# Performance work log

Measured on AMD Instinct MI355X. Metric: run time of the kernel, lower is better.

Reference implementation:

```python
import jax, jax.numpy as jnp
import numpy as np

GRAPH_SIZE = 100000  # == N, used as scalar multiplier on Q


def setup_inputs() -> dict:
    key = jax.random.key(0)
    ks = jax.random.split(key, 10)
    N, D, K, C, S = 100000, 128, 10, 50000, 100
    inp = {
        "seeds_idx_pad": jax.random.randint(ks[0], (1, S), 0, N + 1),  # N = pad row
        "seeds_idx_num": jnp.full((1, 1), 50.0, dtype=jnp.float32),
        "candidates_idx": jax.random.randint(ks[1], (C,), 0, N),
        "all_nodes": jnp.arange(N),
        "mask": jnp.ones((N, 1), dtype=jnp.float32),
        "features": jax.random.normal(ks[2], (N, D), dtype=jnp.float32),
        "neigh_idx": jax.random.randint(ks[3], (N, K), 0, N),
        "W_self": jax.random.normal(ks[4], (D, D), dtype=jnp.float32) * 0.05,
        "W_neigh": jax.random.normal(ks[5], (D, D), dtype=jnp.float32) * 0.05,
        "W1": jax.random.normal(ks[6], (D, D + 1), dtype=jnp.float32) * 0.05,
        "W2": jax.random.normal(ks[7], (D, D + 1), dtype=jnp.float32) * 0.05,
        "W3": jax.random.normal(ks[8], (D, D + 1), dtype=jnp.float32) * 0.05,
    }
    return inp


def _sage(features, neigh_idx, all_nodes, mask, W_self, W_neigh):
    x = features[all_nodes]                 # [N, D]
    nb_mean = features[neigh_idx].mean(axis=1)  # [N, K, D] -> [N, D]
    h = jax.nn.relu(x @ W_self + nb_mean @ W_neigh)
    return h * mask                          # [N, D]


def reference(seeds_idx_pad, seeds_idx_num, candidates_idx, all_nodes, mask,
              features, neigh_idx, W_self, W_neigh, W1, W2, W3):
    D = features.shape[1]
    embedding = _sage(features, neigh_idx, all_nodes, mask, W_self, W_neigh)  # [N, D]
    embedding_pad = jnp.concatenate([embedding, jnp.zeros((1, D), embedding.dtype)], axis=0)
    seeds_emb = embedding_pad[seeds_idx_pad]                  # [1, S, D]
    seeds_mean = jax.nn.sigmoid((seeds_emb.sum(axis=1) / seeds_idx_num) @ W1)  # [1, D+1]
    global_mean = jax.nn.sigmoid(embedding.mean(axis=0)[None, :] @ W2)         # computed but unused, as in source
    candi_emb = jax.nn.sigmoid(embedding[candidates_idx] @ W3)                 # [C, D+1]
    Q = (1.0 - jnp.sum(candi_emb * seeds_mean, axis=1)) * GRAPH_SIZE           # [C]
    return Q
```

## Files before the change

### kernel.cpp

```cpp
#include <hip/hip_runtime.h>

#define D     128
#define DP1   129
#define KN    10
#define GSZ   100000.0f

typedef __attribute__((ext_vector_type(8))) _Float16 f16x8;
typedef __attribute__((ext_vector_type(4))) float f32x4;
typedef __attribute__((ext_vector_type(4))) unsigned uintx4;

#define MFMA16(a, b, c) __builtin_amdgcn_mfma_f32_16x16x32_f16((a), (b), (c), 0, 0, 0)

__device__ __forceinline__ float sigmoidf_(float x) {
    return 1.0f / (1.0f + __expf(-x));
}

__global__ __launch_bounds__(256) void prep_kernel(
    const float* __restrict__ features,
    const float* __restrict__ Wself, const float* __restrict__ Wneigh,
    const float* __restrict__ W3,
    const int*   __restrict__ seeds,
    const float* __restrict__ mask,
    const int*   __restrict__ neigh,
    unsigned short* __restrict__ featb,
    unsigned short* __restrict__ W2T,
    unsigned short* __restrict__ W3T,
    float*          __restrict__ srow,
    int N, int S, int doW)
{
    int b = blockIdx.x;
    const int t = threadIdx.x;

    if (b < S) {
        const int node = seeds[b];
        if (node >= N || node < 0) {
            if (t < D) srow[b * D + t] = 0.f;
            return;
        }
        __shared__ float xs[D], nb[D];
        if (t < D) {
            xs[t] = features[(size_t)node * D + t];
            float a = 0.f;
            #pragma unroll
            for (int k = 0; k < KN; ++k)
                a += features[(size_t)neigh[node * KN + k] * D + t];
            nb[t] = a * (1.0f / KN);
        }
        __syncthreads();
        if (t < D) {
            float h = 0.f;
            #pragma unroll 4
            for (int dp = 0; dp < D; ++dp)
                h = fmaf(xs[dp], Wself[dp * D + t],
                         fmaf(nb[dp], Wneigh[dp * D + t], h));
            srow[b * D + t] = fmaxf(h, 0.f) * mask[node];
        }
        return;
    }
    b -= S;

    if (b < doW * 200) {
        const int u = b * 256 + t;
        if (u < 128 * 256) {
            int n = u >> 8, k = u & 255;
            float v = (k < 128) ? Wself[k * 128 + n] : Wneigh[(k - 128) * 128 + n];
            W2T[n * 256 + k] = __builtin_bit_cast(unsigned short, (_Float16)v);
        } else {
            int w = u - 128 * 256;
            if (w < 144 * 128) {
                int j = w >> 7, k = w & 127;
                float v = (j < DP1) ? W3[k * DP1 + j] : 0.0f;
                W3T[j * 128 + k] = __builtin_bit_cast(unsigned short, (_Float16)v);
            }
        }
        return;
    }
    b -= doW * 200;

    const int i = b * 256 + t;
    const int n8 = N * (D / 8);
    if (i < n8) {
        const float4 a = *(const float4*)(features + (size_t)i * 8);
        const float4 c = *(const float4*)(features + (size_t)i * 8 + 4);
        f16x8 v;
        v[0] = (_Float16)a.x; v[1] = (_Float16)a.y;
        v[2] = (_Float16)a.z; v[3] = (_Float16)a.w;
        v[4] = (_Float16)c.x; v[5] = (_Float16)c.y;
        v[6] = (_Float16)c.z; v[7] = (_Float16)c.w;
        *(f16x8*)(featb + (size_t)i * 8) = v;
    }
}

__global__ __launch_bounds__(256) void sm_kernel(
    const float* __restrict__ srow, int S,
    const float* __restrict__ snum,
    const float* __restrict__ W1,
    float*       __restrict__ smp)
{
    __shared__ float ps[2][D];
    __shared__ float s[D];
    const int t   = threadIdx.x;
    const int col = t & 127;
    const int hf  = t >> 7;
    float a = 0.f;
    for (int b = hf; b < S; b += 2) a += srow[b * D + col];
    ps[hf][col] = a;
    __syncthreads();
    if (t < D) s[t] = (ps[0][t] + ps[1][t]) / snum[0];
    __syncthreads();
    if (t < DP1) {
        float acc = 0.f;
        #pragma unroll 4
        for (int dp = 0; dp < D; ++dp)
            acc = fmaf(s[dp], W1[dp * DP1 + t], acc);
        smp[t] = sigmoidf_(acc);
    } else if (t < 144) {
        smp[t] = 0.0f;
    }
}

__global__ __launch_bounds__(256, 2) void fused_kernel(
    const int*            __restrict__ cand,
    const float*          __restrict__ mask,
    const unsigned short* __restrict__ featb,
    const int*            __restrict__ neigh,
    const unsigned short* __restrict__ W2T,
    const unsigned short* __restrict__ W3T,
    const float*          __restrict__ smp,
    float*                __restrict__ Q,
    int C)
{
    __shared__ unsigned short tile[16][256];
    __shared__ float msk[16];
    __shared__ float qred[4][16];

    const int lane  = threadIdx.x & 63;
    const int wv    = threadIdx.x >> 6;
    const int cbase = blockIdx.x * 16;

    const int g   = lane >> 4;
    const int n15 = lane & 15;

    {
        const int L   = lane & 15;
        const int grp = lane >> 4;
        const int m   = wv * 4 + grp;
        const int cc  = cbase + m;
        const int nd  = cand[(cc < C) ? cc : 0];
        if (L == 0) msk[m] = (cc < C) ? mask[nd] : 0.f;

        int rix[KN];
        #pragma unroll
        for (int k = 0; k < KN; ++k) rix[k] = neigh[nd * KN + k];

        const uintx4 xv = *(const uintx4*)(featb + (size_t)nd * D + L * 8);
        uintx4 vr[KN];
        #pragma unroll
        for (int k = 0; k < KN; ++k)
            vr[k] = *(const uintx4*)(featb + (size_t)rix[k] * D + L * 8);

        f16x8 s8 = __builtin_bit_cast(f16x8, vr[0]);
        #pragma unroll
        for (int k = 1; k < KN; ++k)
            s8 += __builtin_bit_cast(f16x8, vr[k]);
        const f16x8 nb8 = s8 * (f16x8)((_Float16)(1.0f / KN));

        const int sw = (m & 7) << 3;
        unsigned short* tw = &tile[0][0];
        *(uintx4*)(tw + m * 256 + ((L * 8) ^ sw))       = xv;
        *(uintx4*)(tw + m * 256 + ((128 + L * 8) ^ sw)) = __builtin_bit_cast(uintx4, nb8);
    }

    const int swr = (n15 & 7) << 3;
    const unsigned short* tp = &tile[0][0];

    __syncthreads();

    f16x8 afr[8];
    #pragma unroll
    for (int ks = 0; ks < 8; ++ks)
        afr[ks] = *reinterpret_cast<const f16x8*>(tp + n15 * 256 + ((ks * 32 + g * 8) ^ swr));

    f32x4 acc1[2];
    acc1[0] = (f32x4){0.f, 0.f, 0.f, 0.f};
    acc1[1] = (f32x4){0.f, 0.f, 0.f, 0.f};

    #pragma unroll
    for (int ks = 0; ks < 8; ++ks) {
        #pragma unroll
        for (int i = 0; i < 2; ++i) {
            const f16x8 b = *reinterpret_cast<const f16x8*>(
                W2T + ((wv * 2 + i) * 16 + n15) * 256 + ks * 32 + g * 8);
            acc1[i] = MFMA16(afr[ks], b, acc1[i]);
        }
    }

    float mr[4];
    #pragma unroll
    for (int r = 0; r < 4; ++r) mr[r] = msk[g * 4 + r];

    __syncthreads();

    #pragma unroll
    for (int i = 0; i < 2; ++i) {
        const f32x4 v = acc1[i];
        #pragma unroll
        for (int r = 0; r < 4; ++r) {
            const int m2 = g * 4 + r;
            tile[m2][(((wv * 2 + i) * 16 + n15)) ^ ((m2 & 7) << 3)] =
                __builtin_bit_cast(unsigned short, (_Float16)(fmaxf(v[r], 0.f) * mr[r]));
        }
    }
    __syncthreads();

    f16x8 ah[4];
    #pragma unroll
    for (int ks = 0; ks < 4; ++ks)
        ah[ks] = *reinterpret_cast<const f16x8*>(tp + n15 * 256 + ((ks * 32 + g * 8) ^ swr));

    const int jt0 = wv, jt1 = 4 + wv;
    f32x4 acc2[3];
    acc2[0] = (f32x4){0.f, 0.f, 0.f, 0.f};
    acc2[1] = (f32x4){0.f, 0.f, 0.f, 0.f};
    acc2[2] = (f32x4){0.f, 0.f, 0.f, 0.f};

    #pragma unroll
    for (int ks = 0; ks < 4; ++ks) {
        const f16x8 b0 = *reinterpret_cast<const f16x8*>(
            W3T + (jt0 * 16 + n15) * 128 + ks * 32 + g * 8);
        acc2[0] = MFMA16(ah[ks], b0, acc2[0]);
        const f16x8 b1 = *reinterpret_cast<const f16x8*>(
            W3T + (jt1 * 16 + n15) * 128 + ks * 32 + g * 8);
        acc2[1] = MFMA16(ah[ks], b1, acc2[1]);
        if (wv == 0) {
            const f16x8 b2 = *reinterpret_cast<const f16x8*>(
                W3T + (8 * 16 + n15) * 128 + ks * 32 + g * 8);
            acc2[2] = MFMA16(ah[ks], b2, acc2[2]);
        }
    }

    float qp[4] = {0.f, 0.f, 0.f, 0.f};
    {
        const float sm0 = smp[jt0 * 16 + n15];
        const float sm1 = smp[jt1 * 16 + n15];
        #pragma unroll
        for (int r = 0; r < 4; ++r) {
            qp[r] += sm0 * sigmoidf_(acc2[0][r]);
            qp[r] += sm1 * sigmoidf_(acc2[1][r]);
        }
        if (wv == 0) {
            const float sm2 = smp[8 * 16 + n15];
            #pragma unroll
            for (int r = 0; r < 4; ++r)
                qp[r] += sm2 * sigmoidf_(acc2[2][r]);
        }
    }
    #pragma unroll
    for (int off = 8; off >= 1; off >>= 1)
        #pragma unroll
        for (int r = 0; r < 4; ++r)
            qp[r] += __shfl_xor(qp[r], off);

    if (n15 == 0) {
        #pragma unroll
        for (int r = 0; r < 4; ++r)
            qred[wv][g * 4 + r] = qp[r];
    }
    __syncthreads();

    const int t = threadIdx.x;
    if (t < 16) {
        const float s = qred[0][t] + qred[1][t] + qred[2][t] + qred[3][t];
        const int cr = cbase + t;
        if (cr < C) Q[cr] = (1.0f - s) * GSZ;
    }
}

#define MCAND 8
__global__ __launch_bounds__(128) void cand_kernel(
    const int*   __restrict__ cand,
    const float* __restrict__ mask,
    const float* __restrict__ features,
    const int*   __restrict__ neigh,
    const float* __restrict__ Wself,
    const float* __restrict__ Wneigh,
    const float* __restrict__ W3,
    const float* __restrict__ sm,
    float*       __restrict__ Q,
    int C)
{
    const int c0 = blockIdx.x * MCAND;
    const int t  = threadIdx.x;

    __shared__ float z[2 * MCAND][D];
    __shared__ float h[MCAND][D];
    __shared__ float red1[MCAND][D];
    __shared__ float red2[MCAND][D];
    __shared__ float smsh[DP1];

    smsh[t] = sm[t];
    if (t == 0) smsh[D] = sm[D];

    float mskv[MCAND];
    #pragma unroll
    for (int m = 0; m < MCAND; ++m) {
        const int c    = c0 + m;
        const int node = (c < C) ? cand[c] : cand[0];
        mskv[m] = mask[node];
        z[m][t] = features[(size_t)node * D + t];
        float a = 0.f;
        #pragma unroll
        for (int k = 0; k < KN; ++k)
            a += features[(size_t)neigh[node * KN + k] * D + t];
        z[MCAND + m][t] = a * (1.0f / KN);
    }
    __syncthreads();

    float acc[MCAND];
    #pragma unroll
    for (int m = 0; m < MCAND; ++m) acc[m] = 0.f;
    for (int dp = 0; dp < D; dp += 4) {
        const float ws0 = Wself[(dp + 0) * D + t];
        const float ws1 = Wself[(dp + 1) * D + t];
        const float ws2 = Wself[(dp + 2) * D + t];
        const float ws3 = Wself[(dp + 3) * D + t];
        const float wn0 = Wneigh[(dp + 0) * D + t];
        const float wn1 = Wneigh[(dp + 1) * D + t];
        const float wn2 = Wneigh[(dp + 2) * D + t];
        const float wn3 = Wneigh[(dp + 3) * D + t];
        #pragma unroll
        for (int m = 0; m < MCAND; ++m) {
            const float4 xv = *(const float4*)&z[m][dp];
            const float4 nv = *(const float4*)&z[MCAND + m][dp];
            float a = acc[m];
            a = fmaf(xv.x, ws0, a); a = fmaf(xv.y, ws1, a);
            a = fmaf(xv.z, ws2, a); a = fmaf(xv.w, ws3, a);
            a = fmaf(nv.x, wn0, a); a = fmaf(nv.y, wn1, a);
            a = fmaf(nv.z, wn2, a); a = fmaf(nv.w, wn3, a);
            acc[m] = a;
        }
    }
    #pragma unroll
    for (int m = 0; m < MCAND; ++m)
        h[m][t] = fmaxf(acc[m], 0.f) * mskv[m];
    __syncthreads();

    #pragma unroll
    for (int m = 0; m < MCAND; ++m) acc[m] = 0.f;
    for (int dp = 0; dp < D; dp += 4) {
        const float w0 = W3[(dp + 0) * DP1 + t];
        const float w1 = W3[(dp + 1) * DP1 + t];
        const float w2 = W3[(dp + 2) * DP1 + t];
        const float w3 = W3[(dp + 3) * DP1 + t];
        #pragma unroll
        for (int m = 0; m < MCAND; ++m) {
            const float4 hv = *(const float4*)&h[m][dp];
            float a = acc[m];
            a = fmaf(hv.x, w0, a); a = fmaf(hv.y, w1, a);
            a = fmaf(hv.z, w2, a); a = fmaf(hv.w, w3, a);
            acc[m] = a;
        }
    }

    const float w128 = W3[t * DP1 + D];
    const float smt  = smsh[t];
    #pragma unroll
    for (int m = 0; m < MCAND; ++m) {
        red1[m][t] = smt * sigmoidf_(acc[m]);
        red2[m][t] = h[m][t] * w128;
    }
    __syncthreads();

    for (int off = 64; off > 0; off >>= 1) {
        if (t < off) {
            #pragma unroll
            for (int m = 0; m < MCAND; ++m) {
                red1[m][t] += red1[m][t + off];
                red2[m][t] += red2[m][t + off];
            }
        }
        __syncthreads();
    }

    if (t < MCAND && (c0 + t) < C) {
        const float dot = red1[t][0] + smsh[D] * sigmoidf_(red2[t][0]);
        Q[c0 + t] = (1.0f - dot) * GSZ;
    }
}

extern "C" void kernel_launch(void* const* d_in, const int* in_sizes, int n_in,
                              void* d_out, int out_size, void* d_ws, size_t ws_size,
                              hipStream_t stream)
{
    const int*   seeds    = (const int*)  d_in[0];
    const float* snum     = (const float*)d_in[1];
    const int*   cand     = (const int*)  d_in[2];
    const float* mask     = (const float*)d_in[4];
    const float* features = (const float*)d_in[5];
    const int*   neigh    = (const int*)  d_in[6];
    const float* Wself    = (const float*)d_in[7];
    const float* Wneigh   = (const float*)d_in[8];
    const float* W1       = (const float*)d_in[9];
    const float* W3       = (const float*)d_in[11];

    float* Q = (float*)d_out;

    const int S = in_sizes[0];
    const int C = in_sizes[2];
    const int N = in_sizes[3];

    char* ws = (char*)d_ws;
    float*          srow  = (float*)ws;
    float*          smp   = (float*)(ws + 57344);
    unsigned short* W2T   = (unsigned short*)(ws + 65536);
    unsigned short* W3T   = (unsigned short*)(ws + 131072);
    unsigned short* featb = (unsigned short*)(ws + 167936);
    const size_t need = 167936 + (size_t)N * D * 2;
    const bool small_ok = (size_t)S * D * 4 <= 57344;

    if (ws_size >= need && small_ok && (N * D % 2048) == 0) {
        const int nFeatBlk = N * D / 2048;
        prep_kernel<<<S + 200 + nFeatBlk, 256, 0, stream>>>(
            features, Wself, Wneigh, W3, seeds, mask, neigh,
            featb, W2T, W3T, srow, N, S, 1);
        sm_kernel<<<1, 256, 0, stream>>>(srow, S, snum, W1, smp);
        const int nTiles = (C + 15) / 16;
        fused_kernel<<<nTiles, 256, 0, stream>>>(cand, mask, featb,
                                                 neigh, W2T, W3T, smp, Q, C);
    } else {
        prep_kernel<<<S, 256, 0, stream>>>(
            features, Wself, Wneigh, W3, seeds, mask, neigh,
            (unsigned short*)ws, (unsigned short*)ws, (unsigned short*)ws,
            srow, N, S, 0);
        sm_kernel<<<1, 256, 0, stream>>>(srow, S, snum, W1, smp);
        const int nblk = (C + MCAND - 1) / MCAND;
        cand_kernel<<<nblk, 128, 0, stream>>>(cand, mask, features,
                                              neigh, Wself, Wneigh, W3, smp, Q, C);
    }
}
```

Before: 93.92 us.

## Deduplicate candidate nodes via atomic claim table and scatter results to duplicates

Adds a claim table: during prep, each candidate atomically claims its node id so that only one candidate index per distinct node is marked the winner. The fused kernel gathers features and neighbours only for winning candidates and zero-fills the tile rows of the others. A new scatter kernel then copies each winner's Q value to its duplicates. This cuts redundant random gathers for repeated candidates, at the cost of a memset over N ints, atomics in prep, and an extra kernel launch.

```diff
diff --git a/kernel.cpp b/kernel.cpp
--- a/kernel.cpp
+++ b/kernel.cpp
@@ -22,11 +22,13 @@
     const int*   __restrict__ seeds,
     const float* __restrict__ mask,
     const int*   __restrict__ neigh,
+    const int*   __restrict__ cand,
     unsigned short* __restrict__ featb,
     unsigned short* __restrict__ W2T,
     unsigned short* __restrict__ W3T,
     float*          __restrict__ srow,
-    int N, int S, int doW)
+    int*            __restrict__ claim,
+    int N, int S, int C, int doW)
 {
     int b = blockIdx.x;
     const int t = threadIdx.x;
@@ -77,6 +79,17 @@
     }
     b -= doW * 200;
 
+    const int nClaimBlk = (C + 255) / 256;
+    if (b < nClaimBlk) {
+        const int c = b * 256 + t;
+        if (c < C) {
+            const int nd = cand[c];
+            atomicCAS(&claim[nd], 0, c + 1);
+        }
+        return;
+    }
+    b -= nClaimBlk;
+
     const int i = b * 256 + t;
     const int n8 = N * (D / 8);
     if (i < n8) {
@@ -124,6 +137,7 @@
     const float*          __restrict__ mask,
     const unsigned short* __restrict__ featb,
     const int*            __restrict__ neigh,
+    const int*            __restrict__ claim,
     const unsigned short* __restrict__ W2T,
     const unsigned short* __restrict__ W3T,
     const float*          __restrict__ smp,
@@ -146,29 +160,41 @@
         const int grp = lane >> 4;
         const int m   = wv * 4 + grp;
         const int cc  = cbase + m;
-        const int nd  = cand[(cc < C) ? cc : 0];
-        if (L == 0) msk[m] = (cc < C) ? mask[nd] : 0.f;
-
-        int rix[KN];
-        #pragma unroll
-        for (int k = 0; k < KN; ++k) rix[k] = neigh[nd * KN + k];
-
-        const uintx4 xv = *(const uintx4*)(featb + (size_t)nd * D + L * 8);
-        uintx4 vr[KN];
-        #pragma unroll
-        for (int k = 0; k < KN; ++k)
-            vr[k] = *(const uintx4*)(featb + (size_t)rix[k] * D + L * 8);
-
-        f16x8 s8 = __builtin_bit_cast(f16x8, vr[0]);
-        #pragma unroll
-        for (int k = 1; k < KN; ++k)
-            s8 += __builtin_bit_cast(f16x8, vr[k]);
-        const f16x8 nb8 = s8 * (f16x8)((_Float16)(1.0f / KN));
+        int nd = 0;
+        bool win = false;
+        if (cc < C) {
+            nd  = cand[cc];
+            win = (claim[nd] == cc + 1);
+        }
+        if (L == 0) msk[m] = win ? mask[nd] : 0.f;
 
         const int sw = (m & 7) << 3;
         unsigned short* tw = &tile[0][0];
-        *(uintx4*)(tw + m * 256 + ((L * 8) ^ sw))       = xv;
-        *(uintx4*)(tw + m * 256 + ((128 + L * 8) ^ sw)) = __builtin_bit_cast(uintx4, nb8);
+
+        if (win) {
+            int rix[KN];
+            #pragma unroll
+            for (int k = 0; k < KN; ++k) rix[k] = neigh[nd * KN + k];
+
+            const uintx4 xv = *(const uintx4*)(featb + (size_t)nd * D + L * 8);
+            uintx4 vr[KN];
+            #pragma unroll
+            for (int k = 0; k < KN; ++k)
+                vr[k] = *(const uintx4*)(featb + (size_t)rix[k] * D + L * 8);
+
+            f16x8 s8 = __builtin_bit_cast(f16x8, vr[0]);
+            #pragma unroll
+            for (int k = 1; k < KN; ++k)
+                s8 += __builtin_bit_cast(f16x8, vr[k]);
+            const f16x8 nb8 = s8 * (f16x8)((_Float16)(1.0f / KN));
+
+            *(uintx4*)(tw + m * 256 + ((L * 8) ^ sw))       = xv;
+            *(uintx4*)(tw + m * 256 + ((128 + L * 8) ^ sw)) = __builtin_bit_cast(uintx4, nb8);
+        } else {
+            const uintx4 z = {0u, 0u, 0u, 0u};
+            *(uintx4*)(tw + m * 256 + ((L * 8) ^ sw))       = z;
+            *(uintx4*)(tw + m * 256 + ((128 + L * 8) ^ sw)) = z;
+        }
     }
 
     const int swr = (n15 & 7) << 3;
@@ -273,6 +299,19 @@
         const float s = qred[0][t] + qred[1][t] + qred[2][t] + qred[3][t];
         const int cr = cbase + t;
         if (cr < C) Q[cr] = (1.0f - s) * GSZ;
+    }
+}
+
+__global__ __launch_bounds__(256) void scatter_kernel(
+    const int* __restrict__ cand,
+    const int* __restrict__ claim,
+    float*     __restrict__ Q,
+    int C)
+{
+    const int c = blockIdx.x * 256 + threadIdx.x;
+    if (c < C) {
+        const int cw = claim[cand[c]];
+        if (cw > 0) Q[c] = Q[cw - 1];
     }
 }
 
@@ -412,26 +451,34 @@
     char* ws = (char*)d_ws;
     float*          srow  = (float*)ws;
     float*          smp   = (float*)(ws + 57344);
-    unsigned short* W2T   = (unsigned short*)(ws + 65536);
-    unsigned short* W3T   = (unsigned short*)(ws + 131072);
-    unsigned short* featb = (unsigned short*)(ws + 167936);
-    const size_t need = 167936 + (size_t)N * D * 2;
+    int*            claim = (int*)(ws + 58368);
+    size_t off = 58368 + (size_t)N * 4;
+    off = (off + 511) & ~(size_t)511;
+    unsigned short* W2T   = (unsigned short*)(ws + off);
+    unsigned short* W3T   = (unsigned short*)(ws + off + 65536);
+    size_t foff = off + 65536 + 36864;
+    foff = (foff + 511) & ~(size_t)511;
+    unsigned short* featb = (unsigned short*)(ws + foff);
+    const size_t need = foff + (size_t)N * D * 2;
     const bool small_ok = (size_t)S * D * 4 <= 57344;
 
     if (ws_size >= need && small_ok && (N * D % 2048) == 0) {
-        const int nFeatBlk = N * D / 2048;
-        prep_kernel<<<S + 200 + nFeatBlk, 256, 0, stream>>>(
-            features, Wself, Wneigh, W3, seeds, mask, neigh,
-            featb, W2T, W3T, srow, N, S, 1);
+        hipMemsetAsync(claim, 0, (size_t)N * sizeof(int), stream);
+        const int nFeatBlk  = N * D / 2048;
+        const int nClaimBlk = (C + 255) / 256;
+        prep_kernel<<<S + 200 + nClaimBlk + nFeatBlk, 256, 0, stream>>>(
+            features, Wself, Wneigh, W3, seeds, mask, neigh, cand,
+            featb, W2T, W3T, srow, claim, N, S, C, 1);
         sm_kernel<<<1, 256, 0, stream>>>(srow, S, snum, W1, smp);
         const int nTiles = (C + 15) / 16;
-        fused_kernel<<<nTiles, 256, 0, stream>>>(cand, mask, featb,
-                                                 neigh, W2T, W3T, smp, Q, C);
+        fused_kernel<<<nTiles, 256, 0, stream>>>(cand, mask, featb, neigh,
+                                                 claim, W2T, W3T, smp, Q, C);
+        scatter_kernel<<<nClaimBlk, 256, 0, stream>>>(cand, claim, Q, C);
     } else {
         prep_kernel<<<S, 256, 0, stream>>>(
-            features, Wself, Wneigh, W3, seeds, mask, neigh,
+            features, Wself, Wneigh, W3, seeds, mask, neigh, cand,
             (unsigned short*)ws, (unsigned short*)ws, (unsigned short*)ws,
-            srow, N, S, 0);
+            srow, (int*)ws, N, S, 0, 0);
         sm_kernel<<<1, 256, 0, stream>>>(srow, S, snum, W1, smp);
         const int nblk = (C + MCAND - 1) / MCAND;
         cand_kernel<<<nblk, 128, 0, stream>>>(cand, mask, features,
```

Measured after the change: 103.0 us. 9.6% more time.
